# Kernel optimization log

Measured on AMD Instinct MI355X. Metric: run time of the kernel, lower is better.

The kernel has to match this reference:

```python
import jax, jax.numpy as jnp
import numpy as np

N_NODES = 100000
N_EDGES = 2000000
N_GRAPHS = 1000
DIM = 32
NUM_FEATURES = 7
NUM_CLASSES = 2
BN_EPS = 1e-5


def setup_inputs() -> dict:
    key = jax.random.key(0)
    ks = jax.random.split(key, 24)
    inp = {
        "x": jax.random.normal(ks[0], (N_NODES, NUM_FEATURES), dtype=jnp.float32),
        "edge_index": jax.random.randint(ks[1], (2, N_EDGES), 0, N_NODES, dtype=jnp.int64),
        "batch": jnp.sort(jax.random.randint(ks[2], (N_NODES,), 0, N_GRAPHS, dtype=jnp.int64)),
        "conv1_W1": jax.random.normal(ks[3], (NUM_FEATURES, DIM), dtype=jnp.float32) * 0.3,
        "conv1_b1": jax.random.normal(ks[4], (DIM,), dtype=jnp.float32) * 0.1,
        "conv1_W2": jax.random.normal(ks[5], (DIM, DIM), dtype=jnp.float32) * 0.15,
        "conv1_b2": jax.random.normal(ks[6], (DIM,), dtype=jnp.float32) * 0.1,
        "convs_W1": jax.random.normal(ks[7], (4, DIM, DIM), dtype=jnp.float32) * 0.15,
        "convs_b1": jax.random.normal(ks[8], (4, DIM), dtype=jnp.float32) * 0.1,
        "convs_W2": jax.random.normal(ks[9], (4, DIM, DIM), dtype=jnp.float32) * 0.15,
        "convs_b2": jax.random.normal(ks[10], (4, DIM), dtype=jnp.float32) * 0.1,
        "bn_gamma": jax.random.uniform(ks[11], (5, DIM), dtype=jnp.float32, minval=0.5, maxval=1.5),
        "bn_beta": jax.random.normal(ks[12], (5, DIM), dtype=jnp.float32) * 0.1,
        "bn_mean": jax.random.normal(ks[13], (5, DIM), dtype=jnp.float32) * 0.1,
        "bn_var": jax.random.uniform(ks[14], (5, DIM), dtype=jnp.float32, minval=0.5, maxval=1.5),
        "fc1_W": jax.random.normal(ks[15], (DIM, DIM), dtype=jnp.float32) * 0.15,
        "fc1_b": jax.random.normal(ks[16], (DIM,), dtype=jnp.float32) * 0.1,
        "fc2_W": jax.random.normal(ks[17], (DIM, NUM_CLASSES), dtype=jnp.float32) * 0.15,
        "fc2_b": jax.random.normal(ks[18], (NUM_CLASSES,), dtype=jnp.float32) * 0.1,
    }
    return inp


def _gin_conv(h, src, dst, W1, b1, W2, b2):
    # GINConv with eps=0: nn((1+eps)*x + sum_{j in N(i)} x_j)
    agg = jax.ops.segment_sum(h[src], dst, num_segments=N_NODES)
    z = h + agg
    z = jnp.maximum(z @ W1 + b1, 0.0)
    return z @ W2 + b2


def _bn_eval(h, gamma, beta, mean, var):
    return (h - mean) * jax.lax.rsqrt(var + BN_EPS) * gamma + beta


def reference(x, edge_index, batch,
              conv1_W1, conv1_b1, conv1_W2, conv1_b2,
              convs_W1, convs_b1, convs_W2, convs_b2,
              bn_gamma, bn_beta, bn_mean, bn_var,
              fc1_W, fc1_b, fc2_W, fc2_b):
    src, dst = edge_index[0], edge_index[1]
    h = _gin_conv(x, src, dst, conv1_W1, conv1_b1, conv1_W2, conv1_b2)
    h = jnp.maximum(h, 0.0)
    h = _bn_eval(h, bn_gamma[0], bn_beta[0], bn_mean[0], bn_var[0])
    for i in range(4):  # conv2..conv5
        h = _gin_conv(h, src, dst, convs_W1[i], convs_b1[i], convs_W2[i], convs_b2[i])
        h = jnp.maximum(h, 0.0)
        h = _bn_eval(h, bn_gamma[i + 1], bn_beta[i + 1], bn_mean[i + 1], bn_var[i + 1])
    # global add pool over graphs
    g = jax.ops.segment_sum(h, batch, num_segments=N_GRAPHS)  # [G, DIM]
    g = jnp.maximum(g @ fc1_W + fc1_b, 0.0)
    # dropout: eval mode -> identity
    logits = g @ fc2_W + fc2_b
    return jax.nn.log_softmax(logits, axis=-1)
```

## Files before the change

### kernel.cpp

```cpp
#include <hip/hip_runtime.h>

#define N_NODES  100000
#define N_EDGES  2000000
#define N_GRAPHS 1000
#define NFEAT    7
#define BN_EPS   1e-5f
#define MAXDEG   64

#define BSH      7
#define NBKT     782
#define BCAP     3584
#define E_PER_BLK 4096
#define NGRP     6250

__device__ __forceinline__ unsigned bf16_rne(float f) {
  unsigned u = __float_as_uint(f);
  return (u + 0x7FFFu + ((u >> 16) & 1u)) >> 16;
}
__device__ __forceinline__ float bf_lo(unsigned u) { return __uint_as_float(u << 16); }
__device__ __forceinline__ float bf_hi(unsigned u) { return __uint_as_float(u & 0xFFFF0000u); }

__global__ __launch_bounds__(1024) void b1_bucket(const int* __restrict__ src,
                                                  const int* __restrict__ dst,
                                                  int* __restrict__ gCur,
                                                  unsigned* __restrict__ ebuf) {
  __shared__ int hist[NBKT], base[NBKT];
  int tid = threadIdx.x;
  for (int i = tid; i < NBKT; i += 1024) hist[i] = 0;
  __syncthreads();
  unsigned pk[4];
  int bo[4];
  int e0 = blockIdx.x * E_PER_BLK;
#pragma unroll
  for (int k = 0; k < 4; ++k) {
    int e = e0 + k * 1024 + tid;
    if (e < N_EDGES) {
      int d = dst[e], s = src[e];
      int b = d >> BSH;
      int off = atomicAdd(&hist[b], 1);
      pk[k] = ((unsigned)(d & 127) << 17) | (unsigned)s;
      bo[k] = (b << 17) | off;
    } else {
      bo[k] = -1;
    }
  }
  __syncthreads();
  for (int i = tid; i < NBKT; i += 1024)
    base[i] = hist[i] ? atomicAdd(&gCur[i], hist[i]) : 0;
  __syncthreads();
#pragma unroll
  for (int k = 0; k < 4; ++k) {
    if (bo[k] >= 0) {
      int b = bo[k] >> 17, off = bo[k] & 0x1FFFF;
      int p = base[b] + off;
      if (p < BCAP) ebuf[(size_t)b * BCAP + p] = pk[k];
    }
  }
}

__global__ __launch_bounds__(512) void b2_csr(const unsigned* __restrict__ ebuf,
                                              const int* __restrict__ gCnt,
                                              int* __restrict__ cnt,
                                              int* __restrict__ csr,
                                              int* __restrict__ gmax) {
  __shared__ int hist[128];
  __shared__ int stage[128 * MAXDEG];
  int b = blockIdx.x, tid = threadIdx.x;
  if (tid < 128) hist[tid] = 0;
  for (int i = tid; i < 128 * MAXDEG; i += 512) stage[i] = (b << BSH) + (i >> 6);
  __syncthreads();
  int n = gCnt[b];
  if (n > BCAP) n = BCAP;
  const unsigned* eb = ebuf + (size_t)b * BCAP;
  for (int i = tid; i < n; i += 512) {
    unsigned pk = eb[i];
    int dloc = (int)(pk >> 17);
    int slot = atomicAdd(&hist[dloc], 1);
    if (slot < MAXDEG) stage[(dloc << 6) + slot] = (int)(pk & 0x1FFFFu);
  }
  __syncthreads();
  if (tid < 128) {
    int gnode = (b << BSH) + tid;
    if (gnode < N_NODES) cnt[gnode] = hist[tid];
  }
  if (tid < 8) {
    int mx = 1;
#pragma unroll
    for (int k = 0; k < 16; ++k) {
      int d = hist[tid * 16 + k];
      if (d > 63) d = 63;
      if (d + 1 > mx) mx = d + 1;
    }
    gmax[(b << 3) + tid] = mx;
  }
  const int4* st4 = (const int4*)stage;
  int4* dst4 = (int4*)(csr + (size_t)b * (128 * MAXDEG));
  for (int i = tid; i < 128 * MAXDEG / 4; i += 512) dst4[i] = st4[i];
}

__global__ __launch_bounds__(256) void xcvt_kernel(const float* __restrict__ x,
                                                   unsigned* __restrict__ xc) {
  int i = blockIdx.x * 256 + threadIdx.x;
  if (i >= N_NODES * 4) return;
  int n = i >> 2, p = i & 3;
  float lo = x[n * 7 + 2 * p];
  float hi = (2 * p + 1 < 7) ? x[n * 7 + 2 * p + 1] : 0.f;
  xc[i] = bf16_rne(lo) | (bf16_rne(hi) << 16);
}

__global__ __launch_bounds__(256) void gin1(
    const unsigned short* __restrict__ xc16, const int* __restrict__ cnt,
    const int* __restrict__ csr, const int* __restrict__ gmax,
    const float* __restrict__ W1, const float* __restrict__ b1,
    const float* __restrict__ W2, const float* __restrict__ b2,
    const float* __restrict__ gamma, const float* __restrict__ beta,
    const float* __restrict__ mean, const float* __restrict__ var,
    unsigned short* __restrict__ hout16) {
  __shared__ __align__(16) float zs[4][16][12];
  __shared__ __align__(16) float ts[4][32];
  int tid = threadIdx.x;
  int w = __builtin_amdgcn_readfirstlane(tid >> 6);
  int lane = tid & 63;
  int nl = lane & 15;
  int c  = lane >> 4;
  int half = lane >> 5, j = lane & 31;

  float wr1[4], wr2[16];
#pragma unroll
  for (int i = 0; i < 4; ++i) {
    int k = half * 4 + i;
    wr1[i] = (k < 7) ? W1[k * 32 + j] : 0.f;
  }
#pragma unroll
  for (int i = 0; i < 16; ++i) wr2[i] = W2[(half * 16 + i) * 32 + j];
  float vb1 = b1[j], vb2 = b2[j];
  float sc = gamma[j] * rsqrtf(var[j] + BN_EPS);
  float sh = beta[j] - mean[j] * sc;

  const unsigned* xc32 = (const unsigned*)xc16;

  const int NW = gridDim.x * 4;
  for (int g = blockIdx.x * 4 + w; g < NGRP; g += NW) {
    int node = g * 16 + nl;
    int dcnt = cnt[node];
    if (dcnt > 63) dcnt = 63;
    int dE = dcnt + 1;
    int dmax = __builtin_amdgcn_readfirstlane(gmax[g]);
    int nb = (dmax + 3) >> 2;

    const int* crow = csr + (size_t)node * MAXDEG;
    float a0 = 0.f, a1 = 0.f;

    uint4 i4 = *(const uint4*)crow;
    for (int b = 0; b < nb; ++b) {
      uint4 i4n = i4;
      if (b + 1 < nb) i4n = *(const uint4*)(crow + (b + 1) * 4);
      unsigned v0 = xc32[(size_t)i4.x * 4 + c];
      unsigned v1 = xc32[(size_t)i4.y * 4 + c];
      unsigned v2 = xc32[(size_t)i4.z * 4 + c];
      unsigned v3 = xc32[(size_t)i4.w * 4 + c];
      int s0 = b * 4;
      if (s0 + 0 < dE) { a0 += bf_lo(v0); a1 += bf_hi(v0); }
      if (s0 + 1 < dE) { a0 += bf_lo(v1); a1 += bf_hi(v1); }
      if (s0 + 2 < dE) { a0 += bf_lo(v2); a1 += bf_hi(v2); }
      if (s0 + 3 < dE) { a0 += bf_lo(v3); a1 += bf_hi(v3); }
      i4 = i4n;
    }

    {
      float2 z0 = {a0, a1};
      *(float2*)&zs[w][nl][c * 2] = z0;
    }

    for (int p = 0; p < 16; ++p) {
      int np = g * 16 + p;
      float tp = half ? 0.f : vb1;
      {
        const float4* zp = (const float4*)&zs[w][p][half * 4];
        float4 z0 = zp[0];
        tp = fmaf(z0.x, wr1[0], tp); tp = fmaf(z0.y, wr1[1], tp);
        tp = fmaf(z0.z, wr1[2], tp); tp = fmaf(z0.w, wr1[3], tp);
      }
      tp += __shfl_xor(tp, 32);
      tp = fmaxf(tp, 0.f);
      if (!half) ts[w][j] = tp;

      float op = half ? 0.f : vb2;
      {
        const float4* tpp = (const float4*)&ts[w][half * 16];
        float4 t0 = tpp[0], t1 = tpp[1], t2 = tpp[2], t3 = tpp[3];
        op = fmaf(t0.x, wr2[0], op);  op = fmaf(t0.y, wr2[1], op);
        op = fmaf(t0.z, wr2[2], op);  op = fmaf(t0.w, wr2[3], op);
        op = fmaf(t1.x, wr2[4], op);  op = fmaf(t1.y, wr2[5], op);
        op = fmaf(t1.z, wr2[6], op);  op = fmaf(t1.w, wr2[7], op);
        op = fmaf(t2.x, wr2[8], op);  op = fmaf(t2.y, wr2[9], op);
        op = fmaf(t2.z, wr2[10], op); op = fmaf(t2.w, wr2[11], op);
        op = fmaf(t3.x, wr2[12], op); op = fmaf(t3.y, wr2[13], op);
        op = fmaf(t3.z, wr2[14], op); op = fmaf(t3.w, wr2[15], op);
      }
      op += __shfl_xor(op, 32);
      if (!half) {
        op = fmaxf(op, 0.f) * sc + sh;
        float hi = __shfl(op, j | 1);
        if ((j & 1) == 0) {
          unsigned pk = bf16_rne(op) | (bf16_rne(hi) << 16);
          ((unsigned*)hout16)[np * 16 + (j >> 1)] = pk;
        }
      }
    }
  }
}

__global__ __launch_bounds__(256) void gin_layer32(
    const unsigned short* __restrict__ hin16, const int* __restrict__ cnt,
    const int* __restrict__ csr, const int* __restrict__ gmax,
    const float* __restrict__ W1, const float* __restrict__ b1,
    const float* __restrict__ W2, const float* __restrict__ b2,
    const float* __restrict__ gamma, const float* __restrict__ beta,
    const float* __restrict__ mean, const float* __restrict__ var,
    unsigned short* __restrict__ hout16) {
  __shared__ __align__(16) float zs[4][16][36];
  __shared__ __align__(16) float ts[4][32];
  int tid = threadIdx.x;
  int w = __builtin_amdgcn_readfirstlane(tid >> 6);
  int lane = tid & 63;
  int nl = lane & 15;
  int c  = lane >> 4;
  int half = lane >> 5, j = lane & 31;

  float wr1[16], wr2[16];
#pragma unroll
  for (int i = 0; i < 16; ++i) wr1[i] = W1[(half * 16 + i) * 32 + j];
#pragma unroll
  for (int i = 0; i < 16; ++i) wr2[i] = W2[(half * 16 + i) * 32 + j];
  float vb1 = b1[j], vb2 = b2[j];
  float sc = gamma[j] * rsqrtf(var[j] + BN_EPS);
  float sh = beta[j] - mean[j] * sc;

  const int NW = gridDim.x * 4;
  for (int g = blockIdx.x * 4 + w; g < NGRP; g += NW) {
    int node = g * 16 + nl;
    int dcnt = cnt[node];
    if (dcnt > 63) dcnt = 63;
    int dE = dcnt + 1;
    int dmax = __builtin_amdgcn_readfirstlane(gmax[g]);
    int nb = (dmax + 3) >> 2;

    const int* crow = csr + (size_t)node * MAXDEG;
    float acc[8];
#pragma unroll
    for (int i = 0; i < 8; ++i) acc[i] = 0.f;

    uint4 i4 = *(const uint4*)crow;
    for (int b = 0; b < nb; ++b) {
      uint4 i4n = i4;
      if (b + 1 < nb) i4n = *(const uint4*)(crow + (b + 1) * 4);
      uint4 v0 = *(const uint4*)(hin16 + (size_t)i4.x * 32 + c * 8);
      uint4 v1 = *(const uint4*)(hin16 + (size_t)i4.y * 32 + c * 8);
      uint4 v2 = *(const uint4*)(hin16 + (size_t)i4.z * 32 + c * 8);
      uint4 v3 = *(const uint4*)(hin16 + (size_t)i4.w * 32 + c * 8);
      int s0 = b * 4;
      if (s0 + 0 < dE) {
        acc[0] += bf_lo(v0.x); acc[1] += bf_hi(v0.x);
        acc[2] += bf_lo(v0.y); acc[3] += bf_hi(v0.y);
        acc[4] += bf_lo(v0.z); acc[5] += bf_hi(v0.z);
        acc[6] += bf_lo(v0.w); acc[7] += bf_hi(v0.w);
      }
      if (s0 + 1 < dE) {
        acc[0] += bf_lo(v1.x); acc[1] += bf_hi(v1.x);
        acc[2] += bf_lo(v1.y); acc[3] += bf_hi(v1.y);
        acc[4] += bf_lo(v1.z); acc[5] += bf_hi(v1.z);
        acc[6] += bf_lo(v1.w); acc[7] += bf_hi(v1.w);
      }
      if (s0 + 2 < dE) {
        acc[0] += bf_lo(v2.x); acc[1] += bf_hi(v2.x);
        acc[2] += bf_lo(v2.y); acc[3] += bf_hi(v2.y);
        acc[4] += bf_lo(v2.z); acc[5] += bf_hi(v2.z);
        acc[6] += bf_lo(v2.w); acc[7] += bf_hi(v2.w);
      }
      if (s0 + 3 < dE) {
        acc[0] += bf_lo(v3.x); acc[1] += bf_hi(v3.x);
        acc[2] += bf_lo(v3.y); acc[3] += bf_hi(v3.y);
        acc[4] += bf_lo(v3.z); acc[5] += bf_hi(v3.z);
        acc[6] += bf_lo(v3.w); acc[7] += bf_hi(v3.w);
      }
      i4 = i4n;
    }

    {
      float4 z0 = {acc[0], acc[1], acc[2], acc[3]};
      float4 z1 = {acc[4], acc[5], acc[6], acc[7]};
      *(float4*)&zs[w][nl][c * 8]     = z0;
      *(float4*)&zs[w][nl][c * 8 + 4] = z1;
    }

    for (int p = 0; p < 16; ++p) {
      int np = g * 16 + p;
      float tp = half ? 0.f : vb1;
      {
        const float4* zp = (const float4*)&zs[w][p][half * 16];
        float4 q0 = zp[0], q1 = zp[1], q2 = zp[2], q3 = zp[3];
        tp = fmaf(q0.x, wr1[0], tp);  tp = fmaf(q0.y, wr1[1], tp);
        tp = fmaf(q0.z, wr1[2], tp);  tp = fmaf(q0.w, wr1[3], tp);
        tp = fmaf(q1.x, wr1[4], tp);  tp = fmaf(q1.y, wr1[5], tp);
        tp = fmaf(q1.z, wr1[6], tp);  tp = fmaf(q1.w, wr1[7], tp);
        tp = fmaf(q2.x, wr1[8], tp);  tp = fmaf(q2.y, wr1[9], tp);
        tp = fmaf(q2.z, wr1[10], tp); tp = fmaf(q2.w, wr1[11], tp);
        tp = fmaf(q3.x, wr1[12], tp); tp = fmaf(q3.y, wr1[13], tp);
        tp = fmaf(q3.z, wr1[14], tp); tp = fmaf(q3.w, wr1[15], tp);
      }
      tp += __shfl_xor(tp, 32);
      tp = fmaxf(tp, 0.f);
      if (!half) ts[w][j] = tp;

      float op = half ? 0.f : vb2;
      {
        const float4* tpp = (const float4*)&ts[w][half * 16];
        float4 q0 = tpp[0], q1 = tpp[1], q2 = tpp[2], q3 = tpp[3];
        op = fmaf(q0.x, wr2[0], op);  op = fmaf(q0.y, wr2[1], op);
        op = fmaf(q0.z, wr2[2], op);  op = fmaf(q0.w, wr2[3], op);
        op = fmaf(q1.x, wr2[4], op);  op = fmaf(q1.y, wr2[5], op);
        op = fmaf(q1.z, wr2[6], op);  op = fmaf(q1.w, wr2[7], op);
        op = fmaf(q2.x, wr2[8], op);  op = fmaf(q2.y, wr2[9], op);
        op = fmaf(q2.z, wr2[10], op); op = fmaf(q2.w, wr2[11], op);
        op = fmaf(q3.x, wr2[12], op); op = fmaf(q3.y, wr2[13], op);
        op = fmaf(q3.z, wr2[14], op); op = fmaf(q3.w, wr2[15], op);
      }
      op += __shfl_xor(op, 32);
      if (!half) {
        op = fmaxf(op, 0.f) * sc + sh;
        float hi = __shfl(op, j | 1);
        if ((j & 1) == 0) {
          unsigned pk = bf16_rne(op) | (bf16_rne(hi) << 16);
          ((unsigned*)hout16)[np * 16 + (j >> 1)] = pk;
        }
      }
    }
  }
}

__global__ __launch_bounds__(256) void pool_kernel(const unsigned short* __restrict__ h16,
                                                   const int* __restrict__ batch,
                                                   float* __restrict__ g) {
  __shared__ int s_lo, s_hi;
  __shared__ float red[8][33];
  int gr = blockIdx.x;
  if (threadIdx.x == 0) {
    int lo = 0, hi = N_NODES;
    while (lo < hi) { int m = (lo + hi) >> 1; if (batch[m] < gr) lo = m + 1; else hi = m; }
    s_lo = lo;
  } else if (threadIdx.x == 1) {
    int lo = 0, hi = N_NODES;
    while (lo < hi) { int m = (lo + hi) >> 1; if (batch[m] < gr + 1) lo = m + 1; else hi = m; }
    s_hi = lo;
  }
  __syncthreads();
  int lo = s_lo, hi = s_hi;
  int j = threadIdx.x & 31;
  int nd = threadIdx.x >> 5;
  float acc = 0.f;
  for (int n = lo + nd; n < hi; n += 8)
    acc += __uint_as_float((unsigned)h16[n * 32 + j] << 16);
  red[nd][j] = acc;
  __syncthreads();
  if (threadIdx.x < 32) {
    float s = 0.f;
#pragma unroll
    for (int r = 0; r < 8; ++r) s += red[r][j];
    g[gr * 32 + j] = s;
  }
}

__global__ __launch_bounds__(256) void head_kernel(
    const float* __restrict__ g, const float* __restrict__ W1, const float* __restrict__ b1,
    const float* __restrict__ W2, const float* __restrict__ b2, float* __restrict__ out) {
  __shared__ float sW1[1024], sb1[32];
  __shared__ float sW2[64], sb2[2];
  __shared__ float zb[8][33], tb[8][33], lb[8][2];
  int tid = threadIdx.x;
  for (int i = tid; i < 1024; i += 256) sW1[i] = W1[i];
  if (tid < 64) sW2[tid] = W2[tid];
  if (tid < 32) sb1[tid] = b1[tid];
  if (tid < 2) sb2[tid] = b2[tid];
  int nd = tid >> 5;
  int gr = blockIdx.x * 8 + nd;
  int j = tid & 31;
  __syncthreads();
  float z = (gr < N_GRAPHS) ? g[gr * 32 + j] : 0.f;
  zb[nd][j] = z;
  __syncthreads();
  float t = sb1[j];
#pragma unroll
  for (int k = 0; k < 32; ++k) t = fmaf(zb[nd][k], sW1[k * 32 + j], t);
  t = fmaxf(t, 0.f);
  tb[nd][j] = t;
  __syncthreads();
  if (j < 2) {
    float l = sb2[j];
#pragma unroll
    for (int k = 0; k < 32; ++k) l = fmaf(tb[nd][k], sW2[k * 2 + j], l);
    lb[nd][j] = l;
  }
  __syncthreads();
  if (gr < N_GRAPHS && j < 2) {
    float l0 = lb[nd][0], l1 = lb[nd][1];
    float m = fmaxf(l0, l1);
    float lse = m + logf(expf(l0 - m) + expf(l1 - m));
    out[gr * 2 + j] = lb[nd][j] - lse;
  }
}

extern "C" void kernel_launch(void* const* d_in, const int* in_sizes, int n_in,
                              void* d_out, int out_size, void* d_ws, size_t ws_size,
                              hipStream_t stream) {
  const float* x     = (const float*)d_in[0];
  const int*   eidx  = (const int*)d_in[1];
  const int*   batch = (const int*)d_in[2];
  const float* c1W1  = (const float*)d_in[3];
  const float* c1b1  = (const float*)d_in[4];
  const float* c1W2  = (const float*)d_in[5];
  const float* c1b2  = (const float*)d_in[6];
  const float* csW1  = (const float*)d_in[7];
  const float* csb1  = (const float*)d_in[8];
  const float* csW2  = (const float*)d_in[9];
  const float* csb2  = (const float*)d_in[10];
  const float* bng   = (const float*)d_in[11];
  const float* bnb   = (const float*)d_in[12];
  const float* bnm   = (const float*)d_in[13];
  const float* bnv   = (const float*)d_in[14];
  const float* fc1W  = (const float*)d_in[15];
  const float* fc1b  = (const float*)d_in[16];
  const float* fc2W  = (const float*)d_in[17];
  const float* fc2b  = (const float*)d_in[18];
  float* out = (float*)d_out;

  const int* src = eidx;
  const int* dst = eidx + N_EDGES;

  char* p = (char*)d_ws;
  unsigned short* hA16 = (unsigned short*)p; p += (size_t)N_NODES * 32 * 2;
  unsigned short* hB16 = (unsigned short*)p; p += (size_t)N_NODES * 32 * 2;
  int*      cnt  = (int*)p;      p += (size_t)N_NODES * 4;
  int*      csr  = (int*)p;      p += (size_t)NBKT * 128 * MAXDEG * 4;
  unsigned* ebuf = (unsigned*)p; p += (size_t)NBKT * BCAP * 4;
  int*      gCur = (int*)p;      p += 1024 * 4;
  int*      gmax = (int*)p;      p += (size_t)(NBKT * 8) * 4;
  float*    g    = (float*)p;    p += (size_t)N_GRAPHS * 32 * 4;
  unsigned* xc = ebuf;

  (void)hipMemsetAsync(gCur, 0, 1024 * 4, stream);
  b1_bucket<<<(N_EDGES + E_PER_BLK - 1) / E_PER_BLK, 1024, 0, stream>>>(src, dst, gCur, ebuf);
  b2_csr<<<NBKT, 512, 0, stream>>>(ebuf, gCur, cnt, csr, gmax);

  xcvt_kernel<<<(N_NODES * 4 + 255) / 256, 256, 0, stream>>>(x, xc);

  gin1<<<(NGRP + 3) / 4, 256, 0, stream>>>(
      (const unsigned short*)xc, cnt, csr, gmax, c1W1, c1b1, c1W2, c1b2,
      bng, bnb, bnm, bnv, hA16);

  unsigned short* cur = hA16;
  unsigned short* nxt = hB16;
  for (int i = 0; i < 4; ++i) {
    gin_layer32<<<(NGRP + 3) / 4, 256, 0, stream>>>(
        cur, cnt, csr, gmax,
        csW1 + (size_t)i * 1024, csb1 + (size_t)i * 32,
        csW2 + (size_t)i * 1024, csb2 + (size_t)i * 32,
        bng + (size_t)(i + 1) * 32, bnb + (size_t)(i + 1) * 32,
        bnm + (size_t)(i + 1) * 32, bnv + (size_t)(i + 1) * 32, nxt);
    unsigned short* tmp = cur; cur = nxt; nxt = tmp;
  }

  pool_kernel<<<N_GRAPHS, 256, 0, stream>>>(cur, batch, g);
  head_kernel<<<(N_GRAPHS + 7) / 8, 256, 0, stream>>>(g, fc1W, fc1b, fc2W, fc2b, out);
}
```

Before: 341.9 us.

## Replace per-node scalar FMA MLP with split-bf16 MFMA matrix ops

The per-group 16-node MLP in gin_layer32, previously a 16-iteration loop of scalar FMAs and cross-lane shuffles, is now done with 16x16x32 bf16 MFMA instructions. Activations and weights are each split into high and low bf16 parts, and three MFMAs per output tile recover near-fp32 precision. Results pass through LDS to transpose layouts, and each lane writes one 16-byte store. This removes heavy VALU and shuffle work from the compute phase, at the cost of extra MFMAs, LDS round trips and a small precision change.

New measurement: 313.2 us. 1.09x faster.

```diff
diff --git a/kernel.cpp b/kernel.cpp
--- a/kernel.cpp
+++ b/kernel.cpp
@@ -19,6 +19,9 @@
 }
 __device__ __forceinline__ float bf_lo(unsigned u) { return __uint_as_float(u << 16); }
 __device__ __forceinline__ float bf_hi(unsigned u) { return __uint_as_float(u & 0xFFFF0000u); }
+
+typedef __bf16 bf16x8 __attribute__((ext_vector_type(8)));
+typedef float  f32x4  __attribute__((ext_vector_type(4)));
 
 __global__ __launch_bounds__(1024) void b1_bucket(const int* __restrict__ src,
                                                   const int* __restrict__ dst,
@@ -219,23 +222,37 @@
     const float* __restrict__ gamma, const float* __restrict__ beta,
     const float* __restrict__ mean, const float* __restrict__ var,
     unsigned short* __restrict__ hout16) {
-  __shared__ __align__(16) float zs[4][16][36];
-  __shared__ __align__(16) float ts[4][32];
+  __shared__ __align__(16) float ts[4][16][36];
   int tid = threadIdx.x;
   int w = __builtin_amdgcn_readfirstlane(tid >> 6);
   int lane = tid & 63;
   int nl = lane & 15;
-  int c  = lane >> 4;
-  int half = lane >> 5, j = lane & 31;
-
-  float wr1[16], wr2[16];
-#pragma unroll
-  for (int i = 0; i < 16; ++i) wr1[i] = W1[(half * 16 + i) * 32 + j];
-#pragma unroll
-  for (int i = 0; i < 16; ++i) wr2[i] = W2[(half * 16 + i) * 32 + j];
-  float vb1 = b1[j], vb2 = b2[j];
-  float sc = gamma[j] * rsqrtf(var[j] + BN_EPS);
-  float sh = beta[j] - mean[j] * sc;
+  int q  = lane >> 4;
+
+  bf16x8 w1ah, w1al, w1bh, w1bl, w2ah, w2al, w2bh, w2bl;
+#pragma unroll
+  for (int i = 0; i < 8; ++i) {
+    float f;
+    __bf16 h;
+    f = W1[(q * 8 + i) * 32 + nl];       h = (__bf16)f;
+    w1ah[i] = h; w1al[i] = (__bf16)(f - (float)h);
+    f = W1[(q * 8 + i) * 32 + 16 + nl];  h = (__bf16)f;
+    w1bh[i] = h; w1bl[i] = (__bf16)(f - (float)h);
+    f = W2[(q * 8 + i) * 32 + nl];       h = (__bf16)f;
+    w2ah[i] = h; w2al[i] = (__bf16)(f - (float)h);
+    f = W2[(q * 8 + i) * 32 + 16 + nl];  h = (__bf16)f;
+    w2bh[i] = h; w2bl[i] = (__bf16)(f - (float)h);
+  }
+  float vb1a = b1[nl], vb1b = b1[16 + nl];
+  float vb2a = b2[nl], vb2b = b2[16 + nl];
+  f32x4 cb1a = {vb1a, vb1a, vb1a, vb1a};
+  f32x4 cb1b = {vb1b, vb1b, vb1b, vb1b};
+  f32x4 cb2a = {vb2a, vb2a, vb2a, vb2a};
+  f32x4 cb2b = {vb2b, vb2b, vb2b, vb2b};
+  float sc0 = gamma[nl] * rsqrtf(var[nl] + BN_EPS);
+  float sh0 = beta[nl] - mean[nl] * sc0;
+  float sc1 = gamma[16 + nl] * rsqrtf(var[16 + nl] + BN_EPS);
+  float sh1 = beta[16 + nl] - mean[16 + nl] * sc1;
 
   const int NW = gridDim.x * 4;
   for (int g = blockIdx.x * 4 + w; g < NGRP; g += NW) {
@@ -255,10 +272,10 @@
     for (int b = 0; b < nb; ++b) {
       uint4 i4n = i4;
       if (b + 1 < nb) i4n = *(const uint4*)(crow + (b + 1) * 4);
-      uint4 v0 = *(const uint4*)(hin16 + (size_t)i4.x * 32 + c * 8);
-      uint4 v1 = *(const uint4*)(hin16 + (size_t)i4.y * 32 + c * 8);
-      uint4 v2 = *(const uint4*)(hin16 + (size_t)i4.z * 32 + c * 8);
-      uint4 v3 = *(const uint4*)(hin16 + (size_t)i4.w * 32 + c * 8);
+      uint4 v0 = *(const uint4*)(hin16 + (size_t)i4.x * 32 + q * 8);
+      uint4 v1 = *(const uint4*)(hin16 + (size_t)i4.y * 32 + q * 8);
+      uint4 v2 = *(const uint4*)(hin16 + (size_t)i4.z * 32 + q * 8);
+      uint4 v3 = *(const uint4*)(hin16 + (size_t)i4.w * 32 + q * 8);
       int s0 = b * 4;
       if (s0 + 0 < dE) {
         acc[0] += bf_lo(v0.x); acc[1] += bf_hi(v0.x);
@@ -287,54 +304,68 @@
       i4 = i4n;
     }
 
+    bf16x8 af, afl;
+#pragma unroll
+    for (int i = 0; i < 8; ++i) {
+      __bf16 h = (__bf16)acc[i];
+      af[i] = h;
+      afl[i] = (__bf16)(acc[i] - (float)h);
+    }
+
+    f32x4 t0 = __builtin_amdgcn_mfma_f32_16x16x32_bf16(af,  w1ah, cb1a, 0, 0, 0);
+    t0 = __builtin_amdgcn_mfma_f32_16x16x32_bf16(afl, w1ah, t0, 0, 0, 0);
+    t0 = __builtin_amdgcn_mfma_f32_16x16x32_bf16(af,  w1al, t0, 0, 0, 0);
+    f32x4 t1 = __builtin_amdgcn_mfma_f32_16x16x32_bf16(af,  w1bh, cb1b, 0, 0, 0);
+    t1 = __builtin_amdgcn_mfma_f32_16x16x32_bf16(afl, w1bh, t1, 0, 0, 0);
+    t1 = __builtin_amdgcn_mfma_f32_16x16x32_bf16(af,  w1bl, t1, 0, 0, 0);
+#pragma unroll
+    for (int r = 0; r < 4; ++r) {
+      t0[r] = fmaxf(t0[r], 0.f);
+      t1[r] = fmaxf(t1[r], 0.f);
+    }
+#pragma unroll
+    for (int r = 0; r < 4; ++r) {
+      ts[w][q * 4 + r][nl]      = t0[r];
+      ts[w][q * 4 + r][16 + nl] = t1[r];
+    }
+    bf16x8 af2, af2l;
     {
-      float4 z0 = {acc[0], acc[1], acc[2], acc[3]};
-      float4 z1 = {acc[4], acc[5], acc[6], acc[7]};
-      *(float4*)&zs[w][nl][c * 8]     = z0;
-      *(float4*)&zs[w][nl][c * 8 + 4] = z1;
-    }
-
-    for (int p = 0; p < 16; ++p) {
-      int np = g * 16 + p;
-      float tp = half ? 0.f : vb1;
-      {
-        const float4* zp = (const float4*)&zs[w][p][half * 16];
-        float4 q0 = zp[0], q1 = zp[1], q2 = zp[2], q3 = zp[3];
-        tp = fmaf(q0.x, wr1[0], tp);  tp = fmaf(q0.y, wr1[1], tp);
-        tp = fmaf(q0.z, wr1[2], tp);  tp = fmaf(q0.w, wr1[3], tp);
-        tp = fmaf(q1.x, wr1[4], tp);  tp = fmaf(q1.y, wr1[5], tp);
-        tp = fmaf(q1.z, wr1[6], tp);  tp = fmaf(q1.w, wr1[7], tp);
-        tp = fmaf(q2.x, wr1[8], tp);  tp = fmaf(q2.y, wr1[9], tp);
-        tp = fmaf(q2.z, wr1[10], tp); tp = fmaf(q2.w, wr1[11], tp);
-        tp = fmaf(q3.x, wr1[12], tp); tp = fmaf(q3.y, wr1[13], tp);
-        tp = fmaf(q3.z, wr1[14], tp); tp = fmaf(q3.w, wr1[15], tp);
-      }
-      tp += __shfl_xor(tp, 32);
-      tp = fmaxf(tp, 0.f);
-      if (!half) ts[w][j] = tp;
-
-      float op = half ? 0.f : vb2;
-      {
-        const float4* tpp = (const float4*)&ts[w][half * 16];
-        float4 q0 = tpp[0], q1 = tpp[1], q2 = tpp[2], q3 = tpp[3];
-        op = fmaf(q0.x, wr2[0], op);  op = fmaf(q0.y, wr2[1], op);
-        op = fmaf(q0.z, wr2[2], op);  op = fmaf(q0.w, wr2[3], op);
-        op = fmaf(q1.x, wr2[4], op);  op = fmaf(q1.y, wr2[5], op);
-        op = fmaf(q1.z, wr2[6], op);  op = fmaf(q1.w, wr2[7], op);
-        op = fmaf(q2.x, wr2[8], op);  op = fmaf(q2.y, wr2[9], op);
-        op = fmaf(q2.z, wr2[10], op); op = fmaf(q2.w, wr2[11], op);
-        op = fmaf(q3.x, wr2[12], op); op = fmaf(q3.y, wr2[13], op);
-        op = fmaf(q3.z, wr2[14], op); op = fmaf(q3.w, wr2[15], op);
-      }
-      op += __shfl_xor(op, 32);
-      if (!half) {
-        op = fmaxf(op, 0.f) * sc + sh;
-        float hi = __shfl(op, j | 1);
-        if ((j & 1) == 0) {
-          unsigned pk = bf16_rne(op) | (bf16_rne(hi) << 16);
-          ((unsigned*)hout16)[np * 16 + (j >> 1)] = pk;
-        }
-      }
+      float4 r0 = *(const float4*)&ts[w][nl][q * 8];
+      float4 r1 = *(const float4*)&ts[w][nl][q * 8 + 4];
+      float tv[8] = {r0.x, r0.y, r0.z, r0.w, r1.x, r1.y, r1.z, r1.w};
+#pragma unroll
+      for (int i = 0; i < 8; ++i) {
+        __bf16 h = (__bf16)tv[i];
+        af2[i] = h;
+        af2l[i] = (__bf16)(tv[i] - (float)h);
+      }
+    }
+
+    f32x4 o0 = __builtin_amdgcn_mfma_f32_16x16x32_bf16(af2,  w2ah, cb2a, 0, 0, 0);
+    o0 = __builtin_amdgcn_mfma_f32_16x16x32_bf16(af2l, w2ah, o0, 0, 0, 0);
+    o0 = __builtin_amdgcn_mfma_f32_16x16x32_bf16(af2,  w2al, o0, 0, 0, 0);
+    f32x4 o1 = __builtin_amdgcn_mfma_f32_16x16x32_bf16(af2,  w2bh, cb2b, 0, 0, 0);
+    o1 = __builtin_amdgcn_mfma_f32_16x16x32_bf16(af2l, w2bh, o1, 0, 0, 0);
+    o1 = __builtin_amdgcn_mfma_f32_16x16x32_bf16(af2,  w2bl, o1, 0, 0, 0);
+#pragma unroll
+    for (int r = 0; r < 4; ++r) {
+      o0[r] = fmaxf(o0[r], 0.f) * sc0 + sh0;
+      o1[r] = fmaxf(o1[r], 0.f) * sc1 + sh1;
+    }
+#pragma unroll
+    for (int r = 0; r < 4; ++r) {
+      ts[w][q * 4 + r][nl]      = o0[r];
+      ts[w][q * 4 + r][16 + nl] = o1[r];
+    }
+    {
+      float4 f0 = *(const float4*)&ts[w][nl][q * 8];
+      float4 f1 = *(const float4*)&ts[w][nl][q * 8 + 4];
+      uint4 st;
+      st.x = bf16_rne(f0.x) | (bf16_rne(f0.y) << 16);
+      st.y = bf16_rne(f0.z) | (bf16_rne(f0.w) << 16);
+      st.z = bf16_rne(f1.x) | (bf16_rne(f1.y) << 16);
+      st.w = bf16_rne(f1.z) | (bf16_rne(f1.w) << 16);
+      *(uint4*)(hout16 + (size_t)node * 32 + q * 8) = st;
     }
   }
 }
```
